# Performance work log

Measured on AMD Instinct MI355X. Metric: run time of the kernel, lower is better.

Reference implementation:

```python
import jax, jax.numpy as jnp
import numpy as np

N_NODES = 50000
N_EDGES = 800000
NFEAT = 128
NHID = 128
BN_EPS = 1e-5


def setup_inputs() -> dict:
    key = jax.random.key(0)
    ks = jax.random.split(key, 8)
    x = jax.random.normal(ks[0], (N_NODES, NFEAT), dtype=jnp.float32)
    edge_index = jax.random.randint(ks[1], (2, N_EDGES), 0, N_NODES, dtype=jnp.int64)
    # Linear weights in torch layout [out, in]; scaled like kaiming-ish init.
    W1 = jax.random.normal(ks[2], (NHID, NFEAT), dtype=jnp.float32) / np.sqrt(NFEAT)
    b1 = jax.random.normal(ks[3], (NHID,), dtype=jnp.float32) * 0.01
    gamma = jnp.ones((NHID,), dtype=jnp.float32)
    beta = jnp.zeros((NHID,), dtype=jnp.float32)
    W2 = jax.random.normal(ks[4], (NHID, NHID), dtype=jnp.float32) / np.sqrt(NHID)
    b2 = jax.random.normal(ks[5], (NHID,), dtype=jnp.float32) * 0.01
    return {"x": x, "edge_index": edge_index, "W1": W1, "b1": b1,
            "gamma": gamma, "beta": beta, "W2": W2, "b2": b2}


def reference(x, edge_index, W1, b1, gamma, beta, W2, b2):
    # GINConv, eps = 0: h = (1 + eps) * x + sum_{j in N(i)} x_j
    src, dst = edge_index[0], edge_index[1]
    agg = x + jax.ops.segment_sum(x[src], dst, num_segments=N_NODES)  # [N, nfeat]
    # MLP: Linear -> ReLU -> BatchNorm1d (training stats) -> Linear
    h = jnp.maximum(agg @ W1.T + b1, 0.0)                             # [N, nhid]
    mean = jnp.mean(h, axis=0)
    var = jnp.var(h, axis=0)  # biased variance, as torch BN uses for normalization
    h = (h - mean) * jax.lax.rsqrt(var + BN_EPS) * gamma + beta
    return h @ W2.T + b2
```

## Files before the change

kernel.cpp:

```cpp
#include <hip/hip_runtime.h>

#define N_NODES 50000
#define N_EDGES 800000
#define NF 128
#define BN_EPS 1e-5f
#define G_ROWS 32
#define GBLOCKS ((N_NODES + G_ROWS - 1) / G_ROWS)
#define NB 1568
#define AP 136
#define HP 132
#define CAP 32
#define OVFCAP 8192
#define NSLICE 8
#define SLICE_N (N_NODES / NSLICE)
#define SC_BLK 1024
#define CV_BLK 512
#define NCHUNK ((N_EDGES + 255) / 256)

typedef __attribute__((ext_vector_type(8))) short short8;
typedef __attribute__((ext_vector_type(4))) float f32x4;

__device__ __forceinline__ unsigned short f2bf(float f) {
    union { float f; unsigned int i; } v; v.f = f;
    unsigned int r = (v.i + 0x7fffu + ((v.i >> 16) & 1u)) >> 16;
    return (unsigned short)r;
}
__device__ __forceinline__ float bf2f(unsigned short u) {
    union { unsigned int i; float f; } v; v.i = ((unsigned int)u) << 16; return v.f;
}
__device__ __forceinline__ float bflo(unsigned int u) { return bf2f((unsigned short)(u & 0xffffu)); }
__device__ __forceinline__ float bfhi(unsigned int u) { return bf2f((unsigned short)(u >> 16)); }

#define SETUP_C (N_NODES * NF / 4)
#define SETUP_P (128 * 128)

__global__ __launch_bounds__(256) void scatter_build(
    const int* __restrict__ ei,
    int* __restrict__ counts, int* __restrict__ ovfcnt,
    int* __restrict__ ovf, int* __restrict__ bucket,
    const float* __restrict__ x, unsigned short* __restrict__ xb,
    const float* __restrict__ W1, const float* __restrict__ W2,
    unsigned short* __restrict__ Wb1, unsigned short* __restrict__ Wb2,
    int do_convert) {
    int b = blockIdx.x;
    int t = threadIdx.x;
    if (b < SC_BLK) {
        int sl = b & 7;
        int g = b >> 3;
        int lo = sl * SLICE_N;
        int hi = lo + SLICE_N;
        for (int chunk = g; chunk < NCHUNK; chunk += SC_BLK / 8) {
            int e = chunk * 256 + t;
            if (e < N_EDGES) {
                int dst = ei[N_EDGES + e];
                int src = ei[e];
                if (dst >= lo && dst < hi) {
                    int k = atomicAdd(&counts[dst], 1);
                    if (k < CAP) {
                        bucket[dst * CAP + k] = src;
                    } else {
                        int o = atomicAdd(ovfcnt, 1);
                        if (o < OVFCAP) { ovf[2 * o] = dst; ovf[2 * o + 1] = src; }
                    }
                }
            }
        }
    } else {
        int i0 = (b - SC_BLK) * 256 + t;
        int stride = CV_BLK * 256;
        if (do_convert) {
            for (int i = i0; i < SETUP_C; i += stride) {
                float4 v = ((const float4*)x)[i];
                ushort4 u;
                u.x = f2bf(v.x); u.y = f2bf(v.y); u.z = f2bf(v.z); u.w = f2bf(v.w);
                ((ushort4*)xb)[i] = u;
            }
        }
        for (int i = i0; i < SETUP_P; i += stride) {
            Wb1[i] = f2bf(W1[i]);
            Wb2[i] = f2bf(W2[i]);
        }
    }
}

__global__ __launch_bounds__(256, 6) void fused_gather_gemm1_bf16(
    const unsigned short* __restrict__ xb,
    const int* __restrict__ counts,
    const int* __restrict__ bucket,
    const int* __restrict__ ovfcnt,
    const int* __restrict__ ovf,
    const unsigned short* __restrict__ Wb,
    const float* __restrict__ b1,
    unsigned short* __restrict__ buf,
    float* __restrict__ P) {
    __shared__ __align__(16) char smem[G_ROWS * HP * 4];
    unsigned short (*At)[AP] = (unsigned short (*)[AP])smem;
    float (*Ht)[HP] = (float (*)[HP])smem;

    int t = threadIdx.x;
    int wave = t >> 6, lane = t & 63;
    int base = blockIdx.x * G_ROWS;
    int nrows = N_NODES - base; if (nrows > G_ROWS) nrows = G_ROWS;

    const unsigned int* x2 = (const unsigned int*)xb;
    int novf = *ovfcnt; if (novf > OVFCAP) novf = OVFCAP;

    for (int nn = 0; nn < 8; nn++) {
        int r = wave * 8 + nn;
        int node = base + r;
        unsigned int packed = 0u;
        if (node < N_NODES) {
            unsigned int u = x2[(size_t)node * 64 + lane];
            float ax = bflo(u), ay = bfhi(u);
            int deg = counts[node];
            int cnt = deg < CAP ? deg : CAP;
            const int* bkt = bucket + (size_t)node * CAP;
            int e = 0;
            for (; e + 15 < cnt; e += 16) {
                unsigned int uu[16];
#pragma unroll
                for (int k = 0; k < 16; k++) uu[k] = x2[(size_t)bkt[e + k] * 64 + lane];
#pragma unroll
                for (int k = 0; k < 16; k++) { ax += bflo(uu[k]); ay += bfhi(uu[k]); }
            }
            for (; e + 3 < cnt; e += 4) {
                unsigned int u0 = x2[(size_t)bkt[e] * 64 + lane];
                unsigned int u1 = x2[(size_t)bkt[e + 1] * 64 + lane];
                unsigned int u2 = x2[(size_t)bkt[e + 2] * 64 + lane];
                unsigned int u3 = x2[(size_t)bkt[e + 3] * 64 + lane];
                ax += bflo(u0) + bflo(u1) + bflo(u2) + bflo(u3);
                ay += bfhi(u0) + bfhi(u1) + bfhi(u2) + bfhi(u3);
            }
            for (; e < cnt; e++) {
                unsigned int u0 = x2[(size_t)bkt[e] * 64 + lane];
                ax += bflo(u0);
                ay += bfhi(u0);
            }
            if (deg > CAP) {
                for (int o = 0; o < novf; o++) {
                    if (ovf[2 * o] == node) {
                        unsigned int u0 = x2[(size_t)ovf[2 * o + 1] * 64 + lane];
                        ax += bflo(u0);
                        ay += bfhi(u0);
                    }
                }
            }
            packed = ((unsigned int)f2bf(ay) << 16) | (unsigned int)f2bf(ax);
        }
        ((unsigned int*)&At[r][0])[lane] = packed;
    }
    __syncthreads();

    int m0 = (wave & 1) * 16;
    int n0 = (wave >> 1) * 64;
    int l15 = lane & 15, q = lane >> 4;

    f32x4 acc[4];
#pragma unroll
    for (int i = 0; i < 4; i++) acc[i] = (f32x4){0.f, 0.f, 0.f, 0.f};

#pragma unroll
    for (int kc = 0; kc < 4; kc++) {
        short8 a = *((const short8*)&At[m0 + l15][kc * 32 + q * 8]);
#pragma unroll
        for (int tile = 0; tile < 4; tile++) {
            short8 b = *((const short8*)(Wb + (size_t)(n0 + 16 * tile + l15) * 128 + kc * 32 + q * 8));
            acc[tile] = __builtin_amdgcn_mfma_f32_16x16x32_bf16(a, b, acc[tile], 0, 0, 0);
        }
    }
    __syncthreads();

#pragma unroll
    for (int tile = 0; tile < 4; tile++) {
        int col = n0 + 16 * tile + l15;
        float bias = b1[col];
#pragma unroll
        for (int reg = 0; reg < 4; reg++) {
            int row = q * 4 + reg;
            Ht[m0 + row][col] = fmaxf(acc[tile][reg] + bias, 0.f);
        }
    }
    __syncthreads();

    for (int i = t; i < G_ROWS * 32; i += 256) {
        int r = i >> 5, c4 = i & 31;
        int row = base + r;
        if (row < N_NODES) {
            float4 v = *((const float4*)&Ht[r][c4 * 4]);
            ushort4 u;
            u.x = f2bf(v.x); u.y = f2bf(v.y); u.z = f2bf(v.z); u.w = f2bf(v.w);
            *((ushort4*)(buf + (size_t)row * NF + c4 * 4)) = u;
        }
    }

    {
        int f = t & 127;
        bool issq = (t >= 128);
        float s = 0.f;
        for (int r = 0; r < nrows; r++) {
            float v = Ht[r][f];
            s += issq ? v * v : v;
        }
        P[(size_t)t * NB + blockIdx.x] = s;
    }
}

__global__ __launch_bounds__(256) void bn_reduce(const float* __restrict__ P,
                                                 const float* __restrict__ gamma,
                                                 const float* __restrict__ beta,
                                                 float* __restrict__ ab) {
    __shared__ float s1[256], s2[256];
    int f = blockIdx.x;
    int j = threadIdx.x;
    float a = 0.f, b = 0.f;
    for (int k = j; k < GBLOCKS; k += 256) {
        a += P[(size_t)f * NB + k];
        b += P[(size_t)(128 + f) * NB + k];
    }
    s1[j] = a; s2[j] = b;
    __syncthreads();
    for (int off = 128; off > 0; off >>= 1) {
        if (j < off) { s1[j] += s1[j + off]; s2[j] += s2[j + off]; }
        __syncthreads();
    }
    if (j == 0) {
        float mean = s1[0] * (1.0f / N_NODES);
        float var = s2[0] * (1.0f / N_NODES) - mean * mean;
        float rstd = rsqrtf(var + BN_EPS);
        float aa = gamma[f] * rstd;
        float cc = beta[f] - mean * aa;
        ab[f] = aa;
        ab[128 + f] = cc;
    }
}

__global__ __launch_bounds__(256) void gemm2_bf16(
    const unsigned short* __restrict__ buf,
    const unsigned short* __restrict__ Wb,
    const float* __restrict__ b2,
    const float* __restrict__ ab,
    float* __restrict__ out) {
    __shared__ __align__(16) char smem[G_ROWS * HP * 4];
    unsigned short (*At)[AP] = (unsigned short (*)[AP])smem;
    float (*Ht)[HP] = (float (*)[HP])smem;

    int t = threadIdx.x;
    int base = blockIdx.x * G_ROWS;
    int nrows = N_NODES - base; if (nrows > G_ROWS) nrows = G_ROWS;

    for (int i = t; i < G_ROWS * 32; i += 256) {
        int r = i >> 5, c4 = i & 31;
        ushort4 u = make_ushort4(0, 0, 0, 0);
        if (r < nrows) {
            ushort4 hv = *((const ushort4*)(buf + (size_t)(base + r) * NF + c4 * 4));
            float4 av = ((const float4*)ab)[c4];
            float4 cv = ((const float4*)(ab + 128))[c4];
            u.x = f2bf(bf2f(hv.x) * av.x + cv.x);
            u.y = f2bf(bf2f(hv.y) * av.y + cv.y);
            u.z = f2bf(bf2f(hv.z) * av.z + cv.z);
            u.w = f2bf(bf2f(hv.w) * av.w + cv.w);
        }
        *((ushort4*)&At[r][c4 * 4]) = u;
    }
    __syncthreads();

    int wave = t >> 6, lane = t & 63;
    int m0 = (wave & 1) * 16;
    int n0 = (wave >> 1) * 64;
    int l15 = lane & 15, q = lane >> 4;

    f32x4 acc[4];
#pragma unroll
    for (int i = 0; i < 4; i++) acc[i] = (f32x4){0.f, 0.f, 0.f, 0.f};

#pragma unroll
    for (int kc = 0; kc < 4; kc++) {
        short8 a = *((const short8*)&At[m0 + l15][kc * 32 + q * 8]);
#pragma unroll
        for (int tile = 0; tile < 4; tile++) {
            short8 b = *((const short8*)(Wb + (size_t)(n0 + 16 * tile + l15) * 128 + kc * 32 + q * 8));
            acc[tile] = __builtin_amdgcn_mfma_f32_16x16x32_bf16(a, b, acc[tile], 0, 0, 0);
        }
    }
    __syncthreads();

#pragma unroll
    for (int tile = 0; tile < 4; tile++) {
        int col = n0 + 16 * tile + l15;
        float bias = b2[col];
#pragma unroll
        for (int reg = 0; reg < 4; reg++) {
            int row = q * 4 + reg;
            Ht[m0 + row][col] = acc[tile][reg] + bias;
        }
    }
    __syncthreads();

    for (int i = t; i < G_ROWS * 32; i += 256) {
        int r = i >> 5, c4 = i & 31;
        int row = base + r;
        if (row < N_NODES)
            *((float4*)(out + (size_t)row * NF + c4 * 4)) = *((const float4*)&Ht[r][c4 * 4]);
    }
}

__global__ void finalize_bn(const float* __restrict__ stats,
                            const float* __restrict__ gamma,
                            const float* __restrict__ beta,
                            float* __restrict__ ab) {
    int f = threadIdx.x;
    if (f < 128) {
        float mean = stats[f] * (1.0f / N_NODES);
        float var = stats[128 + f] * (1.0f / N_NODES) - mean * mean;
        float rstd = rsqrtf(var + BN_EPS);
        float a = gamma[f] * rstd;
        float c = beta[f] - mean * a;
        ab[f] = a;
        ab[128 + f] = c;
    }
}

__global__ __launch_bounds__(256) void fused_gather_gemm1_f32(
    const float* __restrict__ xv,
    const int* __restrict__ counts,
    const int* __restrict__ bucket,
    const int* __restrict__ ovfcnt,
    const int* __restrict__ ovf,
    const unsigned short* __restrict__ Wb,
    const float* __restrict__ b1,
    float* __restrict__ hout,
    float* __restrict__ stats) {
    __shared__ unsigned short At[G_ROWS][AP];
    __shared__ float Ht[G_ROWS][HP];

    int t = threadIdx.x;
    int wave = t >> 6, lane = t & 63;
    int base = blockIdx.x * G_ROWS;
    int nrows = N_NODES - base; if (nrows > G_ROWS) nrows = G_ROWS;

    const float2* xf2 = (const float2*)xv;
    int novf = *ovfcnt; if (novf > OVFCAP) novf = OVFCAP;

    for (int nn = 0; nn < 8; nn++) {
        int r = wave * 8 + nn;
        int node = base + r;
        float2 acc = make_float2(0.f, 0.f);
        if (node < N_NODES) {
            acc = xf2[(size_t)node * 64 + lane];
            int deg = counts[node];
            int cnt = deg < CAP ? deg : CAP;
            const int* bkt = bucket + (size_t)node * CAP;
            for (int e = 0; e < cnt; e++) {
                float2 v0 = xf2[(size_t)bkt[e] * 64 + lane];
                acc.x += v0.x;
                acc.y += v0.y;
            }
            if (deg > CAP) {
                for (int o = 0; o < novf; o++) {
                    if (ovf[2 * o] == node) {
                        float2 v0 = xf2[(size_t)ovf[2 * o + 1] * 64 + lane];
                        acc.x += v0.x;
                        acc.y += v0.y;
                    }
                }
            }
        }
        unsigned int packed = ((unsigned int)f2bf(acc.y) << 16) | (unsigned int)f2bf(acc.x);
        *((unsigned int*)&At[r][lane * 2]) = packed;
    }
    __syncthreads();

    int m0 = (wave & 1) * 16;
    int n0 = (wave >> 1) * 64;
    int l15 = lane & 15, q = lane >> 4;

    f32x4 acc[4];
#pragma unroll
    for (int i = 0; i < 4; i++) acc[i] = (f32x4){0.f, 0.f, 0.f, 0.f};

#pragma unroll
    for (int kc = 0; kc < 4; kc++) {
        short8 a = *((const short8*)&At[m0 + l15][kc * 32 + q * 8]);
#pragma unroll
        for (int tile = 0; tile < 4; tile++) {
            short8 b = *((const short8*)(Wb + (size_t)(n0 + 16 * tile + l15) * 128 + kc * 32 + q * 8));
            acc[tile] = __builtin_amdgcn_mfma_f32_16x16x32_bf16(a, b, acc[tile], 0, 0, 0);
        }
    }

#pragma unroll
    for (int tile = 0; tile < 4; tile++) {
        int col = n0 + 16 * tile + l15;
        float bias = b1[col];
#pragma unroll
        for (int reg = 0; reg < 4; reg++) {
            int row = q * 4 + reg;
            Ht[m0 + row][col] = fmaxf(acc[tile][reg] + bias, 0.f);
        }
    }
    __syncthreads();

    for (int i = t; i < G_ROWS * 32; i += 256) {
        int r = i >> 5, c4 = i & 31;
        int row = base + r;
        if (row < N_NODES)
            *((float4*)(hout + (size_t)row * NF + c4 * 4)) = *((const float4*)&Ht[r][c4 * 4]);
    }

    if (t < 128) {
        float s = 0.f, sq = 0.f;
        for (int r = 0; r < nrows; r++) {
            float v = Ht[r][t];
            s += v; sq += v * v;
        }
        atomicAdd(&stats[t], s);
        atomicAdd(&stats[128 + t], sq);
    }
}

__global__ __launch_bounds__(256) void gemm2_f32(
    float* __restrict__ h,
    const unsigned short* __restrict__ Wb,
    const float* __restrict__ b2,
    const float* __restrict__ ab) {
    __shared__ unsigned short At[G_ROWS][AP];
    __shared__ float Ht[G_ROWS][HP];

    int t = threadIdx.x;
    int base = blockIdx.x * G_ROWS;
    int nrows = N_NODES - base; if (nrows > G_ROWS) nrows = G_ROWS;

    for (int i = t; i < G_ROWS * 32; i += 256) {
        int r = i >> 5, c4 = i & 31;
        float4 v = make_float4(0.f, 0.f, 0.f, 0.f);
        if (r < nrows) {
            float4 hv = ((const float4*)(h + (size_t)(base + r) * NF))[c4];
            float4 av = ((const float4*)ab)[c4];
            float4 cv = ((const float4*)(ab + 128))[c4];
            v.x = hv.x * av.x + cv.x;
            v.y = hv.y * av.y + cv.y;
            v.z = hv.z * av.z + cv.z;
            v.w = hv.w * av.w + cv.w;
        }
        ushort4 u;
        u.x = f2bf(v.x); u.y = f2bf(v.y); u.z = f2bf(v.z); u.w = f2bf(v.w);
        *((ushort4*)&At[r][c4 * 4]) = u;
    }
    __syncthreads();

    int wave = t >> 6, lane = t & 63;
    int m0 = (wave & 1) * 16;
    int n0 = (wave >> 1) * 64;
    int l15 = lane & 15, q = lane >> 4;

    f32x4 acc[4];
#pragma unroll
    for (int i = 0; i < 4; i++) acc[i] = (f32x4){0.f, 0.f, 0.f, 0.f};

#pragma unroll
    for (int kc = 0; kc < 4; kc++) {
        short8 a = *((const short8*)&At[m0 + l15][kc * 32 + q * 8]);
#pragma unroll
        for (int tile = 0; tile < 4; tile++) {
            short8 b = *((const short8*)(Wb + (size_t)(n0 + 16 * tile + l15) * 128 + kc * 32 + q * 8));
            acc[tile] = __builtin_amdgcn_mfma_f32_16x16x32_bf16(a, b, acc[tile], 0, 0, 0);
        }
    }

#pragma unroll
    for (int tile = 0; tile < 4; tile++) {
        int col = n0 + 16 * tile + l15;
        float bias = b2[col];
#pragma unroll
        for (int reg = 0; reg < 4; reg++) {
            int row = q * 4 + reg;
            Ht[m0 + row][col] = acc[tile][reg] + bias;
        }
    }
    __syncthreads();

    for (int i = t; i < G_ROWS * 32; i += 256) {
        int r = i >> 5, c4 = i & 31;
        int row = base + r;
        if (row < N_NODES)
            *((float4*)(h + (size_t)row * NF + c4 * 4)) = *((const float4*)&Ht[r][c4 * 4]);
    }
}

extern "C" void kernel_launch(void* const* d_in, const int* in_sizes, int n_in,
                              void* d_out, int out_size, void* d_ws, size_t ws_size,
                              hipStream_t stream) {
    const float* x     = (const float*)d_in[0];
    const int*   ei    = (const int*)d_in[1];
    const float* W1    = (const float*)d_in[2];
    const float* b1    = (const float*)d_in[3];
    const float* gamma = (const float*)d_in[4];
    const float* beta  = (const float*)d_in[5];
    const float* W2    = (const float*)d_in[6];
    const float* b2    = (const float*)d_in[7];

    float* out = (float*)d_out;

    float*          stats    = (float*)d_ws;
    float*          ab       = stats + 256;
    float*          P        = ab + 256;
    unsigned short* Wb1      = (unsigned short*)(P + 256 * NB);
    unsigned short* Wb2      = Wb1 + 128 * 128;
    int*            counts   = (int*)(Wb2 + 128 * 128);
    int*            ovfcnt   = counts + N_NODES;
    int*            ovf      = ovfcnt + 16;
    int*            bucket   = ovf + 2 * OVFCAP;
    unsigned short* xb       = (unsigned short*)(bucket + (size_t)N_NODES * CAP);
    unsigned short* buf      = xb + (size_t)N_NODES * NF;

    size_t need = (size_t)((char*)(buf + (size_t)N_NODES * NF) - (char*)d_ws);
    size_t need_fb = (size_t)((char*)xb - (char*)d_ws);
    bool bf16_path = ws_size >= need;

    if (bf16_path) {
        hipMemsetAsync(counts, 0, (N_NODES + 16) * sizeof(int), stream);
        scatter_build<<<SC_BLK + CV_BLK, 256, 0, stream>>>(
            ei, counts, ovfcnt, ovf, bucket, x, xb, W1, W2, Wb1, Wb2, 1);
        fused_gather_gemm1_bf16<<<GBLOCKS, 256, 0, stream>>>(
            xb, counts, bucket, ovfcnt, ovf, Wb1, b1, buf, P);
        bn_reduce<<<128, 256, 0, stream>>>(P, gamma, beta, ab);
        gemm2_bf16<<<GBLOCKS, 256, 0, stream>>>(buf, Wb2, b2, ab, out);
    } else if (ws_size >= need_fb) {
        hipMemsetAsync(counts, 0, (N_NODES + 16) * sizeof(int), stream);
        hipMemsetAsync(stats, 0, 256 * sizeof(float), stream);
        scatter_build<<<SC_BLK + CV_BLK, 256, 0, stream>>>(
            ei, counts, ovfcnt, ovf, bucket, x, (unsigned short*)0, W1, W2, Wb1, Wb2, 0);
        fused_gather_gemm1_f32<<<GBLOCKS, 256, 0, stream>>>(
            x, counts, bucket, ovfcnt, ovf, Wb1, b1, out, stats);
        finalize_bn<<<1, 128, 0, stream>>>(stats, gamma, beta, ab);
        gemm2_f32<<<GBLOCKS, 256, 0, stream>>>(out, Wb2, b2, ab);
    }
}
```

Before: 201.2 us.

## Fuse gather, GEMM1, BN reduction and GEMM2 into one cooperative persistent kernel

Adds a cooperative megakernel that keeps each block's hidden tile in shared memory across two grid-wide barriers, computes BatchNorm statistics in-grid, then applies the normalization and GEMM2 without writing the intermediate bf16 buffer to global memory. This removes two kernel launches and a full read and write of the hidden activations. In exchange it requires all 1563 blocks to be co-resident (about 7 per CU on 256 CUs) and adds spin-barrier latency. It falls back to the three-kernel path when occupancy or the cooperative launch fails.

Measured after the change: 198.4 us. Within noise of the previous version (-1.4%).

```diff
diff --git a/kernel.cpp b/kernel.cpp
--- a/kernel.cpp
+++ b/kernel.cpp
@@ -83,6 +83,230 @@
     }
 }
 
+__device__ __forceinline__ void gbar(int* cnt, int* flag, int epoch, int nb) {
+    __syncthreads();
+    if (threadIdx.x == 0) {
+        int v = __hip_atomic_fetch_add(cnt, 1, __ATOMIC_ACQ_REL, __HIP_MEMORY_SCOPE_AGENT);
+        if (v == nb - 1) {
+            __hip_atomic_store(cnt, 0, __ATOMIC_RELAXED, __HIP_MEMORY_SCOPE_AGENT);
+            __hip_atomic_store(flag, epoch, __ATOMIC_RELEASE, __HIP_MEMORY_SCOPE_AGENT);
+        } else {
+            while (__hip_atomic_load(flag, __ATOMIC_RELAXED, __HIP_MEMORY_SCOPE_AGENT) < epoch)
+                __builtin_amdgcn_s_sleep(8);
+        }
+    }
+    __syncthreads();
+}
+
+__global__ __launch_bounds__(256, 7) void mega_bf16(
+    const unsigned short* __restrict__ xb,
+    const int* __restrict__ counts,
+    const int* __restrict__ bucket,
+    const int* __restrict__ ovfcnt,
+    const int* __restrict__ ovf,
+    const unsigned short* __restrict__ Wb1,
+    const float* __restrict__ b1,
+    const unsigned short* __restrict__ Wb2,
+    const float* __restrict__ b2,
+    const float* __restrict__ gamma,
+    const float* __restrict__ beta,
+    float* __restrict__ P,
+    float* __restrict__ ab,
+    int* __restrict__ bar,
+    float* __restrict__ out) {
+    __shared__ __align__(16) char smem[G_ROWS * HP * 4];
+    __shared__ __align__(16) float saux[512];
+    unsigned short (*At)[AP] = (unsigned short (*)[AP])smem;
+    float (*Ht)[HP] = (float (*)[HP])smem;
+
+    int t = threadIdx.x;
+    int wave = t >> 6, lane = t & 63;
+    int base = blockIdx.x * G_ROWS;
+    int nrows = N_NODES - base; if (nrows > G_ROWS) nrows = G_ROWS;
+
+    const unsigned int* x2 = (const unsigned int*)xb;
+    int novf = *ovfcnt; if (novf > OVFCAP) novf = OVFCAP;
+
+    for (int nn = 0; nn < 8; nn++) {
+        int r = wave * 8 + nn;
+        int node = base + r;
+        unsigned int packed = 0u;
+        if (node < N_NODES) {
+            unsigned int u = x2[(size_t)node * 64 + lane];
+            float ax = bflo(u), ay = bfhi(u);
+            int deg = counts[node];
+            int cnt = deg < CAP ? deg : CAP;
+            const int* bkt = bucket + (size_t)node * CAP;
+            int e = 0;
+            for (; e + 15 < cnt; e += 16) {
+                unsigned int uu[16];
+#pragma unroll
+                for (int k = 0; k < 16; k++) uu[k] = x2[(size_t)bkt[e + k] * 64 + lane];
+#pragma unroll
+                for (int k = 0; k < 16; k++) { ax += bflo(uu[k]); ay += bfhi(uu[k]); }
+            }
+            for (; e + 3 < cnt; e += 4) {
+                unsigned int u0 = x2[(size_t)bkt[e] * 64 + lane];
+                unsigned int u1 = x2[(size_t)bkt[e + 1] * 64 + lane];
+                unsigned int u2 = x2[(size_t)bkt[e + 2] * 64 + lane];
+                unsigned int u3 = x2[(size_t)bkt[e + 3] * 64 + lane];
+                ax += bflo(u0) + bflo(u1) + bflo(u2) + bflo(u3);
+                ay += bfhi(u0) + bfhi(u1) + bfhi(u2) + bfhi(u3);
+            }
+            for (; e < cnt; e++) {
+                unsigned int u0 = x2[(size_t)bkt[e] * 64 + lane];
+                ax += bflo(u0);
+                ay += bfhi(u0);
+            }
+            if (deg > CAP) {
+                for (int o = 0; o < novf; o++) {
+                    if (ovf[2 * o] == node) {
+                        unsigned int u0 = x2[(size_t)ovf[2 * o + 1] * 64 + lane];
+                        ax += bflo(u0);
+                        ay += bfhi(u0);
+                    }
+                }
+            }
+            packed = ((unsigned int)f2bf(ay) << 16) | (unsigned int)f2bf(ax);
+        }
+        ((unsigned int*)&At[r][0])[lane] = packed;
+    }
+    __syncthreads();
+
+    {
+        int m0 = (wave & 1) * 16;
+        int n0 = (wave >> 1) * 64;
+        int l15 = lane & 15, q = lane >> 4;
+        f32x4 acc[4];
+#pragma unroll
+        for (int i = 0; i < 4; i++) acc[i] = (f32x4){0.f, 0.f, 0.f, 0.f};
+#pragma unroll
+        for (int kc = 0; kc < 4; kc++) {
+            short8 a = *((const short8*)&At[m0 + l15][kc * 32 + q * 8]);
+#pragma unroll
+            for (int tile = 0; tile < 4; tile++) {
+                short8 b = *((const short8*)(Wb1 + (size_t)(n0 + 16 * tile + l15) * 128 + kc * 32 + q * 8));
+                acc[tile] = __builtin_amdgcn_mfma_f32_16x16x32_bf16(a, b, acc[tile], 0, 0, 0);
+            }
+        }
+        __syncthreads();
+#pragma unroll
+        for (int tile = 0; tile < 4; tile++) {
+            int col = n0 + 16 * tile + l15;
+            float bias = b1[col];
+#pragma unroll
+            for (int reg = 0; reg < 4; reg++) {
+                int row = q * 4 + reg;
+                Ht[m0 + row][col] = fmaxf(acc[tile][reg] + bias, 0.f);
+            }
+        }
+    }
+    __syncthreads();
+
+    {
+        int f = t & 127;
+        bool issq = (t >= 128);
+        float s = 0.f;
+        for (int r = 0; r < nrows; r++) {
+            float v = Ht[r][f];
+            s += issq ? v * v : v;
+        }
+        __hip_atomic_store(&P[(size_t)t * NB + blockIdx.x], s,
+                           __ATOMIC_RELAXED, __HIP_MEMORY_SCOPE_AGENT);
+    }
+
+    gbar(bar, bar + 1, 1, (int)gridDim.x);
+
+    if (blockIdx.x < 128) {
+        int f = blockIdx.x;
+        float a = 0.f, b = 0.f;
+        for (int k = t; k < GBLOCKS; k += 256) {
+            a += __hip_atomic_load(&P[(size_t)f * NB + k], __ATOMIC_RELAXED, __HIP_MEMORY_SCOPE_AGENT);
+            b += __hip_atomic_load(&P[(size_t)(128 + f) * NB + k], __ATOMIC_RELAXED, __HIP_MEMORY_SCOPE_AGENT);
+        }
+        saux[t] = a; saux[256 + t] = b;
+        __syncthreads();
+        for (int off = 128; off > 0; off >>= 1) {
+            if (t < off) { saux[t] += saux[t + off]; saux[256 + t] += saux[256 + t + off]; }
+            __syncthreads();
+        }
+        if (t == 0) {
+            float mean = saux[0] * (1.0f / N_NODES);
+            float var = saux[256] * (1.0f / N_NODES) - mean * mean;
+            float rstd = rsqrtf(var + BN_EPS);
+            float aa = gamma[f] * rstd;
+            float cc = beta[f] - mean * aa;
+            __hip_atomic_store(&ab[f], aa, __ATOMIC_RELAXED, __HIP_MEMORY_SCOPE_AGENT);
+            __hip_atomic_store(&ab[128 + f], cc, __ATOMIC_RELAXED, __HIP_MEMORY_SCOPE_AGENT);
+        }
+    }
+
+    gbar(bar, bar + 1, 2, (int)gridDim.x);
+
+    saux[t] = __hip_atomic_load(&ab[t], __ATOMIC_RELAXED, __HIP_MEMORY_SCOPE_AGENT);
+    __syncthreads();
+
+    {
+        float4 hv[4];
+#pragma unroll
+        for (int it = 0; it < 4; it++) {
+            int i = t + it * 256; int r = i >> 5, c4 = i & 31;
+            hv[it] = *((const float4*)&Ht[r][c4 * 4]);
+        }
+        __syncthreads();
+#pragma unroll
+        for (int it = 0; it < 4; it++) {
+            int i = t + it * 256; int r = i >> 5, c4 = i & 31;
+            float4 av = *((const float4*)&saux[c4 * 4]);
+            float4 cv = *((const float4*)&saux[128 + c4 * 4]);
+            ushort4 u;
+            u.x = f2bf(hv[it].x * av.x + cv.x);
+            u.y = f2bf(hv[it].y * av.y + cv.y);
+            u.z = f2bf(hv[it].z * av.z + cv.z);
+            u.w = f2bf(hv[it].w * av.w + cv.w);
+            *((ushort4*)&At[r][c4 * 4]) = u;
+        }
+    }
+    __syncthreads();
+
+    {
+        int m0 = (wave & 1) * 16;
+        int n0 = (wave >> 1) * 64;
+        int l15 = lane & 15, q = lane >> 4;
+        f32x4 acc[4];
+#pragma unroll
+        for (int i = 0; i < 4; i++) acc[i] = (f32x4){0.f, 0.f, 0.f, 0.f};
+#pragma unroll
+        for (int kc = 0; kc < 4; kc++) {
+            short8 a = *((const short8*)&At[m0 + l15][kc * 32 + q * 8]);
+#pragma unroll
+            for (int tile = 0; tile < 4; tile++) {
+                short8 b = *((const short8*)(Wb2 + (size_t)(n0 + 16 * tile + l15) * 128 + kc * 32 + q * 8));
+                acc[tile] = __builtin_amdgcn_mfma_f32_16x16x32_bf16(a, b, acc[tile], 0, 0, 0);
+            }
+        }
+        __syncthreads();
+#pragma unroll
+        for (int tile = 0; tile < 4; tile++) {
+            int col = n0 + 16 * tile + l15;
+            float bias = b2[col];
+#pragma unroll
+            for (int reg = 0; reg < 4; reg++) {
+                int row = q * 4 + reg;
+                Ht[m0 + row][col] = acc[tile][reg] + bias;
+            }
+        }
+    }
+    __syncthreads();
+
+    for (int i = t; i < G_ROWS * 32; i += 256) {
+        int r = i >> 5, c4 = i & 31;
+        int row = base + r;
+        if (row < N_NODES)
+            *((float4*)(out + (size_t)row * NF + c4 * 4)) = *((const float4*)&Ht[r][c4 * 4]);
+    }
+}
+
 __global__ __launch_bounds__(256, 6) void fused_gather_gemm1_bf16(
     const unsigned short* __restrict__ xb,
     const int* __restrict__ counts,
@@ -158,7 +382,6 @@
     f32x4 acc[4];
 #pragma unroll
     for (int i = 0; i < 4; i++) acc[i] = (f32x4){0.f, 0.f, 0.f, 0.f};
-
 #pragma unroll
     for (int kc = 0; kc < 4; kc++) {
         short8 a = *((const short8*)&At[m0 + l15][kc * 32 + q * 8]);
@@ -169,7 +392,6 @@
         }
     }
     __syncthreads();
-
 #pragma unroll
     for (int tile = 0; tile < 4; tile++) {
         int col = n0 + 16 * tile + l15;
@@ -272,7 +494,6 @@
     f32x4 acc[4];
 #pragma unroll
     for (int i = 0; i < 4; i++) acc[i] = (f32x4){0.f, 0.f, 0.f, 0.f};
-
 #pragma unroll
     for (int kc = 0; kc < 4; kc++) {
         short8 a = *((const short8*)&At[m0 + l15][kc * 32 + q * 8]);
@@ -283,7 +504,6 @@
         }
     }
     __syncthreads();
-
 #pragma unroll
     for (int tile = 0; tile < 4; tile++) {
         int col = n0 + 16 * tile + l15;
@@ -377,7 +597,6 @@
     f32x4 acc[4];
 #pragma unroll
     for (int i = 0; i < 4; i++) acc[i] = (f32x4){0.f, 0.f, 0.f, 0.f};
-
 #pragma unroll
     for (int kc = 0; kc < 4; kc++) {
         short8 a = *((const short8*)&At[m0 + l15][kc * 32 + q * 8]);
@@ -387,7 +606,6 @@
             acc[tile] = __builtin_amdgcn_mfma_f32_16x16x32_bf16(a, b, acc[tile], 0, 0, 0);
         }
     }
-
 #pragma unroll
     for (int tile = 0; tile < 4; tile++) {
         int col = n0 + 16 * tile + l15;
@@ -456,7 +674,6 @@
     f32x4 acc[4];
 #pragma unroll
     for (int i = 0; i < 4; i++) acc[i] = (f32x4){0.f, 0.f, 0.f, 0.f};
-
 #pragma unroll
     for (int kc = 0; kc < 4; kc++) {
         short8 a = *((const short8*)&At[m0 + l15][kc * 32 + q * 8]);
@@ -466,7 +683,6 @@
             acc[tile] = __builtin_amdgcn_mfma_f32_16x16x32_bf16(a, b, acc[tile], 0, 0, 0);
         }
     }
-
 #pragma unroll
     for (int tile = 0; tile < 4; tile++) {
         int col = n0 + 16 * tile + l15;
@@ -521,10 +737,39 @@
         hipMemsetAsync(counts, 0, (N_NODES + 16) * sizeof(int), stream);
         scatter_build<<<SC_BLK + CV_BLK, 256, 0, stream>>>(
             ei, counts, ovfcnt, ovf, bucket, x, xb, W1, W2, Wb1, Wb2, 1);
-        fused_gather_gemm1_bf16<<<GBLOCKS, 256, 0, stream>>>(
-            xb, counts, bucket, ovfcnt, ovf, Wb1, b1, buf, P);
-        bn_reduce<<<128, 256, 0, stream>>>(P, gamma, beta, ab);
-        gemm2_bf16<<<GBLOCKS, 256, 0, stream>>>(buf, Wb2, b2, ab, out);
+
+        bool mega_ok = false;
+        static int s_occ = -1;
+        if (s_occ < 0) {
+            int o = 0;
+            if (hipOccupancyMaxActiveBlocksPerMultiprocessor(&o, mega_bf16, 256, 0) != hipSuccess)
+                o = 0;
+            s_occ = o;
+        }
+        if (s_occ * 256 >= GBLOCKS) {
+            const unsigned short* a_xb = xb;   const int* a_counts = counts;
+            const int* a_bucket = bucket;      const int* a_ovfcnt = ovfcnt;
+            const int* a_ovf = ovf;            const unsigned short* a_Wb1 = Wb1;
+            const float* a_b1 = b1;            const unsigned short* a_Wb2 = Wb2;
+            const float* a_b2 = b2;            const float* a_gamma = gamma;
+            const float* a_beta = beta;        float* a_P = P;
+            float* a_ab = ab;                  int* a_bar = ovfcnt + 2;
+            float* a_out = out;
+            void* args[] = {
+                (void*)&a_xb, (void*)&a_counts, (void*)&a_bucket, (void*)&a_ovfcnt,
+                (void*)&a_ovf, (void*)&a_Wb1, (void*)&a_b1, (void*)&a_Wb2,
+                (void*)&a_b2, (void*)&a_gamma, (void*)&a_beta, (void*)&a_P,
+                (void*)&a_ab, (void*)&a_bar, (void*)&a_out };
+            hipError_t err = hipLaunchCooperativeKernel(
+                (const void*)mega_bf16, dim3(GBLOCKS), dim3(256), args, 0, stream);
+            mega_ok = (err == hipSuccess);
+        }
+        if (!mega_ok) {
+            fused_gather_gemm1_bf16<<<GBLOCKS, 256, 0, stream>>>(
+                xb, counts, bucket, ovfcnt, ovf, Wb1, b1, buf, P);
+            bn_reduce<<<128, 256, 0, stream>>>(P, gamma, beta, ab);
+            gemm2_bf16<<<GBLOCKS, 256, 0, stream>>>(buf, Wb2, b2, ab, out);
+        }
     } else if (ws_size >= need_fb) {
         hipMemsetAsync(counts, 0, (N_NODES + 16) * sizeof(int), stream);
         hipMemsetAsync(stats, 0, 256 * sizeof(float), stream);
```

## Replace BN partial-sum buffer and reduce kernel with atomics folded into gemm2

Applied to the files above, without the earlier changes.

Each gemm1 block now atomically adds its per-feature sum and sum-of-squares into one of two 256-float accumulators instead of writing a partials array. The separate bn_reduce kernel is removed, and every gemm2 block recomputes the BN scale and shift from these accumulators in shared memory. This drops one kernel launch and the partials traffic. In exchange it adds atomic contention, on 1563 blocks spread over only two slots, and makes the float summation order nondeterministic.

After: 203.1 us. No clear change (+0.9%).

```diff
diff --git a/kernel.cpp b/kernel.cpp
--- a/kernel.cpp
+++ b/kernel.cpp
@@ -6,7 +6,6 @@
 #define BN_EPS 1e-5f
 #define G_ROWS 32
 #define GBLOCKS ((N_NODES + G_ROWS - 1) / G_ROWS)
-#define NB 1568
 #define AP 136
 #define HP 132
 #define CAP 32
@@ -92,7 +91,7 @@
     const unsigned short* __restrict__ Wb,
     const float* __restrict__ b1,
     unsigned short* __restrict__ buf,
-    float* __restrict__ P) {
+    float* __restrict__ Pg) {
     __shared__ __align__(16) char smem[G_ROWS * HP * 4];
     unsigned short (*At)[AP] = (unsigned short (*)[AP])smem;
     float (*Ht)[HP] = (float (*)[HP])smem;
@@ -158,7 +157,6 @@
     f32x4 acc[4];
 #pragma unroll
     for (int i = 0; i < 4; i++) acc[i] = (f32x4){0.f, 0.f, 0.f, 0.f};
-
 #pragma unroll
     for (int kc = 0; kc < 4; kc++) {
         short8 a = *((const short8*)&At[m0 + l15][kc * 32 + q * 8]);
@@ -201,36 +199,7 @@
             float v = Ht[r][f];
             s += issq ? v * v : v;
         }
-        P[(size_t)t * NB + blockIdx.x] = s;
-    }
-}
-
-__global__ __launch_bounds__(256) void bn_reduce(const float* __restrict__ P,
-                                                 const float* __restrict__ gamma,
-                                                 const float* __restrict__ beta,
-                                                 float* __restrict__ ab) {
-    __shared__ float s1[256], s2[256];
-    int f = blockIdx.x;
-    int j = threadIdx.x;
-    float a = 0.f, b = 0.f;
-    for (int k = j; k < GBLOCKS; k += 256) {
-        a += P[(size_t)f * NB + k];
-        b += P[(size_t)(128 + f) * NB + k];
-    }
-    s1[j] = a; s2[j] = b;
-    __syncthreads();
-    for (int off = 128; off > 0; off >>= 1) {
-        if (j < off) { s1[j] += s1[j + off]; s2[j] += s2[j + off]; }
-        __syncthreads();
-    }
-    if (j == 0) {
-        float mean = s1[0] * (1.0f / N_NODES);
-        float var = s2[0] * (1.0f / N_NODES) - mean * mean;
-        float rstd = rsqrtf(var + BN_EPS);
-        float aa = gamma[f] * rstd;
-        float cc = beta[f] - mean * aa;
-        ab[f] = aa;
-        ab[128 + f] = cc;
+        atomicAdd(&Pg[(blockIdx.x & 1) * 256 + t], s);
     }
 }
 
@@ -238,23 +207,39 @@
     const unsigned short* __restrict__ buf,
     const unsigned short* __restrict__ Wb,
     const float* __restrict__ b2,
-    const float* __restrict__ ab,
+    const float* __restrict__ Pg,
+    const float* __restrict__ gamma,
+    const float* __restrict__ beta,
     float* __restrict__ out) {
     __shared__ __align__(16) char smem[G_ROWS * HP * 4];
+    __shared__ float sab[256];
     unsigned short (*At)[AP] = (unsigned short (*)[AP])smem;
     float (*Ht)[HP] = (float (*)[HP])smem;
 
     int t = threadIdx.x;
     int base = blockIdx.x * G_ROWS;
     int nrows = N_NODES - base; if (nrows > G_ROWS) nrows = G_ROWS;
+
+    sab[t] = Pg[t] + Pg[256 + t];
+    __syncthreads();
+    if (t < 128) {
+        float sum = sab[t], sq = sab[128 + t];
+        float mean = sum * (1.0f / N_NODES);
+        float var = sq * (1.0f / N_NODES) - mean * mean;
+        float rstd = rsqrtf(var + BN_EPS);
+        float aa = gamma[t] * rstd;
+        sab[t] = aa;
+        sab[128 + t] = beta[t] - mean * aa;
+    }
+    __syncthreads();
 
     for (int i = t; i < G_ROWS * 32; i += 256) {
         int r = i >> 5, c4 = i & 31;
         ushort4 u = make_ushort4(0, 0, 0, 0);
         if (r < nrows) {
             ushort4 hv = *((const ushort4*)(buf + (size_t)(base + r) * NF + c4 * 4));
-            float4 av = ((const float4*)ab)[c4];
-            float4 cv = ((const float4*)(ab + 128))[c4];
+            float4 av = *((const float4*)&sab[c4 * 4]);
+            float4 cv = *((const float4*)&sab[128 + c4 * 4]);
             u.x = f2bf(bf2f(hv.x) * av.x + cv.x);
             u.y = f2bf(bf2f(hv.y) * av.y + cv.y);
             u.z = f2bf(bf2f(hv.z) * av.z + cv.z);
@@ -272,7 +257,6 @@
     f32x4 acc[4];
 #pragma unroll
     for (int i = 0; i < 4; i++) acc[i] = (f32x4){0.f, 0.f, 0.f, 0.f};
-
 #pragma unroll
     for (int kc = 0; kc < 4; kc++) {
         short8 a = *((const short8*)&At[m0 + l15][kc * 32 + q * 8]);
@@ -283,7 +267,6 @@
         }
     }
     __syncthreads();
-
 #pragma unroll
     for (int tile = 0; tile < 4; tile++) {
         int col = n0 + 16 * tile + l15;
@@ -377,7 +360,6 @@
     f32x4 acc[4];
 #pragma unroll
     for (int i = 0; i < 4; i++) acc[i] = (f32x4){0.f, 0.f, 0.f, 0.f};
-
 #pragma unroll
     for (int kc = 0; kc < 4; kc++) {
         short8 a = *((const short8*)&At[m0 + l15][kc * 32 + q * 8]);
@@ -387,7 +369,6 @@
             acc[tile] = __builtin_amdgcn_mfma_f32_16x16x32_bf16(a, b, acc[tile], 0, 0, 0);
         }
     }
-
 #pragma unroll
     for (int tile = 0; tile < 4; tile++) {
         int col = n0 + 16 * tile + l15;
@@ -456,7 +437,6 @@
     f32x4 acc[4];
 #pragma unroll
     for (int i = 0; i < 4; i++) acc[i] = (f32x4){0.f, 0.f, 0.f, 0.f};
-
 #pragma unroll
     for (int kc = 0; kc < 4; kc++) {
         short8 a = *((const short8*)&At[m0 + l15][kc * 32 + q * 8]);
@@ -466,7 +446,6 @@
             acc[tile] = __builtin_amdgcn_mfma_f32_16x16x32_bf16(a, b, acc[tile], 0, 0, 0);
         }
     }
-
 #pragma unroll
     for (int tile = 0; tile < 4; tile++) {
         int col = n0 + 16 * tile + l15;
@@ -503,12 +482,12 @@
 
     float*          stats    = (float*)d_ws;
     float*          ab       = stats + 256;
-    float*          P        = ab + 256;
-    unsigned short* Wb1      = (unsigned short*)(P + 256 * NB);
+    unsigned short* Wb1      = (unsigned short*)(ab + 256);
     unsigned short* Wb2      = Wb1 + 128 * 128;
     int*            counts   = (int*)(Wb2 + 128 * 128);
     int*            ovfcnt   = counts + N_NODES;
-    int*            ovf      = ovfcnt + 16;
+    float*          Pg       = (float*)(ovfcnt + 16);
+    int*            ovf      = (int*)(Pg + 512);
     int*            bucket   = ovf + 2 * OVFCAP;
     unsigned short* xb       = (unsigned short*)(bucket + (size_t)N_NODES * CAP);
     unsigned short* buf      = xb + (size_t)N_NODES * NF;
@@ -518,15 +497,14 @@
     bool bf16_path = ws_size >= need;
 
     if (bf16_path) {
-        hipMemsetAsync(counts, 0, (N_NODES + 16) * sizeof(int), stream);
+        hipMemsetAsync(counts, 0, (N_NODES + 16 + 512) * sizeof(int), stream);
         scatter_build<<<SC_BLK + CV_BLK, 256, 0, stream>>>(
             ei, counts, ovfcnt, ovf, bucket, x, xb, W1, W2, Wb1, Wb2, 1);
         fused_gather_gemm1_bf16<<<GBLOCKS, 256, 0, stream>>>(
-            xb, counts, bucket, ovfcnt, ovf, Wb1, b1, buf, P);
-        bn_reduce<<<128, 256, 0, stream>>>(P, gamma, beta, ab);
-        gemm2_bf16<<<GBLOCKS, 256, 0, stream>>>(buf, Wb2, b2, ab, out);
+            xb, counts, bucket, ovfcnt, ovf, Wb1, b1, buf, Pg);
+        gemm2_bf16<<<GBLOCKS, 256, 0, stream>>>(buf, Wb2, b2, Pg, gamma, beta, out);
     } else if (ws_size >= need_fb) {
-        hipMemsetAsync(counts, 0, (N_NODES + 16) * sizeof(int), stream);
+        hipMemsetAsync(counts, 0, (N_NODES + 16 + 512) * sizeof(int), stream);
         hipMemsetAsync(stats, 0, 256 * sizeof(float), stream);
         scatter_build<<<SC_BLK + CV_BLK, 256, 0, stream>>>(
             ei, counts, ovfcnt, ovf, bucket, x, (unsigned short*)0, W1, W2, Wb1, Wb2, 0);
```
